# Kernel tuning notes

Hardware: AMD Instinct MI355X
Metric: run time of the kernel (lower is better)

Reference implementation:

```python
import jax, jax.numpy as jnp
import numpy as np

B, N, D = 8, 4096, 256
T = 768          # text_dim
E = 4            # num_experts
K = 2            # top_k
GS = 64          # grid_size = img_size // patch_size
WS = 8           # swin window size
NH = 4           # swin heads
MODES = 16       # fno modes
HID = 4 * D      # mlp hidden


def setup_inputs() -> dict:
    key = jax.random.key(0)
    ks = jax.random.split(key, 40)
    rn = lambda k, s, sc=0.02: jax.random.normal(k, s, jnp.float32) * sc
    return {
        "x": jax.random.normal(ks[0], (B, N, D), jnp.float32),
        "text_embedding": jax.random.normal(ks[1], (B, T), jnp.float32),
        # TopKGating: Linear(D+T->D), ReLU, Linear(D->E)
        "g1_w": rn(ks[2], (D, D + T)), "g1_b": jnp.zeros((D,), jnp.float32),
        "g2_w": rn(ks[3], (E, D)), "g2_b": jnp.zeros((E,), jnp.float32),
        # FNOExpert: SpectralConv2d complex weights (real/imag) + 1x1 conv
        "fno_w1r": rn(ks[4], (D, D, MODES, MODES), 1.0 / D), "fno_w1i": rn(ks[5], (D, D, MODES, MODES), 1.0 / D),
        "fno_w2r": rn(ks[6], (D, D, MODES, MODES), 1.0 / D), "fno_w2i": rn(ks[7], (D, D, MODES, MODES), 1.0 / D),
        "fno_cw": rn(ks[8], (D, D)), "fno_cb": jnp.zeros((D,), jnp.float32),
        # MLPExpert #1
        "m1_w1": rn(ks[9], (HID, D)), "m1_b1": jnp.zeros((HID,), jnp.float32),
        "m1_w2": rn(ks[10], (D, HID)), "m1_b2": jnp.zeros((D,), jnp.float32),
        # WindowAttentionExpert
        "a_ln1w": jnp.ones((D,), jnp.float32), "a_ln1b": jnp.zeros((D,), jnp.float32),
        "a_qkvw": rn(ks[11], (3 * D, D)), "a_qkvb": jnp.zeros((3 * D,), jnp.float32),
        "a_ow": rn(ks[12], (D, D)), "a_ob": jnp.zeros((D,), jnp.float32),
        "a_ln2w": jnp.ones((D,), jnp.float32), "a_ln2b": jnp.zeros((D,), jnp.float32),
        "a_mw1": rn(ks[13], (HID, D)), "a_mb1": jnp.zeros((HID,), jnp.float32),
        "a_mw2": rn(ks[14], (D, HID)), "a_mb2": jnp.zeros((D,), jnp.float32),
        # MLPExpert #2 (extra expert to reach num_experts=4)
        "m2_w1": rn(ks[15], (HID, D)), "m2_b1": jnp.zeros((HID,), jnp.float32),
        "m2_w2": rn(ks[16], (D, HID)), "m2_b2": jnp.zeros((D,), jnp.float32),
    }


def _gelu(v):
    return jax.nn.gelu(v, approximate=False)


def _ln(v, g, b, eps=1e-5):
    m = v.mean(-1, keepdims=True)
    var = ((v - m) ** 2).mean(-1, keepdims=True)
    return (v - m) * jax.lax.rsqrt(var + eps) * g + b


def reference(x, text_embedding, g1_w, g1_b, g2_w, g2_b,
              fno_w1r, fno_w1i, fno_w2r, fno_w2i, fno_cw, fno_cb,
              m1_w1, m1_b1, m1_w2, m1_b2,
              a_ln1w, a_ln1b, a_qkvw, a_qkvb, a_ow, a_ob,
              a_ln2w, a_ln2b, a_mw1, a_mb1, a_mw2, a_mb2,
              m2_w1, m2_b1, m2_w2, m2_b2):
    Bb, Nn, Dd = x.shape

    # ---- TopKGating ----
    feat = jnp.concatenate([x.mean(axis=1), text_embedding], axis=1)   # [B, D+T]
    h = jax.nn.relu(feat @ g1_w.T + g1_b)
    logits = h @ g2_w.T + g2_b                                         # [B, E]
    vals, idx = jax.lax.top_k(logits, K)
    w = jax.nn.softmax(vals, axis=1)                                   # [B, K]
    # per-(sample, expert) combine weight; indices are constants
    combine = (w[..., None] * jax.nn.one_hot(idx, E, dtype=x.dtype)).sum(axis=1)  # [B, E]

    # ---- Expert 0: FNO ----
    def fno(v):
        xg = v.transpose(0, 2, 1).reshape(Bb, Dd, GS, GS)              # [B, D, H, W]
        xft = jnp.fft.rfft2(xg)                                        # [B, D, H, W//2+1]
        w1 = fno_w1r + 1j * fno_w1i
        w2 = fno_w2r + 1j * fno_w2i
        lo = jnp.einsum('bixy,ioxy->boxy', xft[:, :, :MODES, :MODES], w1)
        hi = jnp.einsum('bixy,ioxy->boxy', xft[:, :, -MODES:, :MODES], w2)
        out_ft = jnp.zeros_like(xft)
        out_ft = out_ft.at[:, :, :MODES, :MODES].set(lo)
        out_ft = out_ft.at[:, :, -MODES:, :MODES].set(hi)
        x1 = jnp.fft.irfft2(out_ft, s=(GS, GS))
        x2 = jnp.einsum('bihw,oi->bohw', xg, fno_cw) + fno_cb[None, :, None, None]
        out = _gelu(x1 + x2)
        return out.reshape(Bb, Dd, Nn).transpose(0, 2, 1) + v

    # ---- MLP experts ----
    def mlp(v, w1, b1, w2, b2):
        return _gelu(v @ w1.T + b1) @ w2.T + b2 + v

    # ---- Expert 2: window attention ----
    def win_attn(v):
        xs = _ln(v, a_ln1w, a_ln1b).reshape(Bb, GS, GS, Dd)
        nw = GS // WS
        xw = xs.reshape(Bb, nw, WS, nw, WS, Dd).transpose(0, 1, 3, 2, 4, 5)
        xw = xw.reshape(-1, WS * WS, Dd)                               # [B*nw*nw, L, D]
        qkv = xw @ a_qkvw.T + a_qkvb
        q, k, vv = jnp.split(qkv, 3, axis=-1)
        dh = Dd // NH
        heads = lambda t: t.reshape(-1, WS * WS, NH, dh).transpose(0, 2, 1, 3)
        q, k, vv = heads(q), heads(k), heads(vv)
        attn = jax.nn.softmax(q @ k.transpose(0, 1, 3, 2) / jnp.sqrt(jnp.float32(dh)), axis=-1)
        o = (attn @ vv).transpose(0, 2, 1, 3).reshape(-1, WS * WS, Dd) @ a_ow.T + a_ob
        o = o.reshape(Bb, nw, nw, WS, WS, Dd).transpose(0, 1, 3, 2, 4, 5).reshape(Bb, Nn, Dd)
        v2 = v + o
        return v2 + (_gelu(_ln(v2, a_ln2w, a_ln2b) @ a_mw1.T + a_mb1) @ a_mw2.T + a_mb2)

    outs = [fno(x),
            mlp(x, m1_w1, m1_b1, m1_w2, m1_b2),
            win_attn(x),
            mlp(x, m2_w1, m2_b1, m2_w2, m2_b2)]
    final = sum(combine[:, e, None, None] * outs[e] for e in range(E))
    return final, w
```

## Files before the change

### kernel.cpp

```cpp
#include <hip/hip_runtime.h>
#include <math.h>

#define BB 8
#define NN 4096
#define DDIM 256
#define TT 768
#define BND (BB*NN*DDIM)

typedef unsigned short ushort_t;
typedef short bf16x8 __attribute__((ext_vector_type(8)));
typedef float f32x4 __attribute__((ext_vector_type(4)));

__device__ __forceinline__ float gelu_f(float v){
    return 0.5f * v * (1.0f + erff(v * 0.70710678118654752f));
}
__device__ __forceinline__ ushort_t f2bf(float f){
    union { float f; unsigned int u; } v; v.f = f;
    unsigned int u = v.u;
    u += 0x7FFFu + ((u >> 16) & 1u);
    return (ushort_t)(u >> 16);
}
__device__ __forceinline__ float bf2f(ushort_t h){
    union { unsigned int u; float f; } v; v.u = ((unsigned int)h) << 16;
    return v.f;
}
__device__ __forceinline__ float pk_re(unsigned int p){
    union { unsigned int u; float f; } v; v.u = p << 16; return v.f;
}
__device__ __forceinline__ float pk_im(unsigned int p){
    union { unsigned int u; float f; } v; v.u = p & 0xffff0000u; return v.f;
}
#define GLOAD16(gp, lp) __builtin_amdgcn_global_load_lds( \
    (__attribute__((address_space(1))) const void*)(gp),  \
    (__attribute__((address_space(3))) void*)(lp), 16, 0, 0)

__global__ __launch_bounds__(256) void k_meanA(const float* __restrict__ x, float* __restrict__ partial){
    int c = blockIdx.x, b = blockIdx.y, t = threadIdx.x;
    const float* p = x + ((size_t)b*NN + c*256)*DDIM + t;
    float s0=0,s1=0,s2=0,s3=0;
    for (int n=0;n<256;n+=4){
        s0 += p[(size_t)n*DDIM];
        s1 += p[(size_t)(n+1)*DDIM];
        s2 += p[(size_t)(n+2)*DDIM];
        s3 += p[(size_t)(n+3)*DDIM];
    }
    partial[((size_t)b*16 + c)*256 + t] = (s0+s1)+(s2+s3);
}

__global__ __launch_bounds__(256) void k_gate1(const float* __restrict__ partial, const float* __restrict__ text,
    const float* __restrict__ g1w, const float* __restrict__ g1b, float* __restrict__ hs){
    int d = blockIdx.x, t = threadIdx.x;
    int w = t >> 6, lane = t & 63;
    float xm[BB];
    #pragma unroll
    for (int b=0;b<BB;++b){
        float s = 0.f;
        #pragma unroll
        for (int c=0;c<16;++c) s += partial[((size_t)b*16 + c)*256 + t];
        xm[b] = s * (1.0f/NN);
    }
    const float* wrow = g1w + (size_t)d*(DDIM+TT);
    float w0 = wrow[t], w1 = wrow[256+t], w2 = wrow[512+t], w3 = wrow[768+t];
    float acc[BB];
    #pragma unroll
    for (int b=0;b<BB;++b){
        const float* tx = text + (size_t)b*TT;
        acc[b] = xm[b]*w0 + tx[t]*w1 + tx[256+t]*w2 + tx[512+t]*w3;
    }
    #pragma unroll
    for (int b=0;b<BB;++b)
        for (int off=32; off; off>>=1) acc[b] += __shfl_down(acc[b], off);
    __shared__ float red[BB][4];
    if (lane==0)
        #pragma unroll
        for (int b=0;b<BB;++b) red[b][w] = acc[b];
    __syncthreads();
    if (t < BB){
        float s = red[t][0]+red[t][1]+red[t][2]+red[t][3] + g1b[d];
        hs[t*DDIM + d] = fmaxf(s, 0.0f);
    }
}

__global__ __launch_bounds__(64) void k_gate2(const float* __restrict__ hs,
    const float* __restrict__ g2w, const float* __restrict__ g2b,
    float* __restrict__ combine, float* __restrict__ wout){
    __shared__ float lg[BB][4];
    int t = threadIdx.x;
    if (t < 32){
        int b = t>>2, e = t&3;
        float a = g2b[e];
        const float* w2 = g2w + e*DDIM;
        const float* h = hs + b*DDIM;
        for (int o=0;o<DDIM;o+=4)
            a += h[o]*w2[o] + h[o+1]*w2[o+1] + h[o+2]*w2[o+2] + h[o+3]*w2[o+3];
        lg[b][e] = a;
    }
    __syncthreads();
    if (t < BB){
        int b = t;
        int i1=0; float v1=lg[b][0];
        for (int e=1;e<4;++e){ if (lg[b][e] > v1){ v1=lg[b][e]; i1=e; } }
        int i2=0; float v2=-3.0e38f; bool found=false;
        for (int e=0;e<4;++e){ if (e==i1) continue; if (!found || lg[b][e] > v2){ v2=lg[b][e]; i2=e; found=true; } }
        float e2 = expf(v2 - v1);
        float inv = 1.0f/(1.0f + e2);
        float w0 = inv, w1 = e2*inv;
        float cv[4] = {0.f,0.f,0.f,0.f};
        cv[i1] = w0; cv[i2] = w1;
        for (int e=0;e<4;++e) combine[b*4+e] = cv[e];
        wout[b*2+0] = w0; wout[b*2+1] = w1;
    }
}

__global__ __launch_bounds__(256) void k_cvtw(
    const float* __restrict__ s0, const float* __restrict__ s1, const float* __restrict__ s2,
    const float* __restrict__ s3, const float* __restrict__ s4, const float* __restrict__ s5,
    const float* __restrict__ s6, const float* __restrict__ s7, const float* __restrict__ s8,
    ushort_t* __restrict__ dst){
    const int off[10] = {0,196608,262144,524288,786432,1048576,1310720,1572864,1835008,1900544};
    const float* srcs[9] = {s0,s1,s2,s3,s4,s5,s6,s7,s8};
    int i = (blockIdx.x*256 + threadIdx.x)*8;
    if (i >= 1900544) return;
    int seg = 0;
    #pragma unroll
    for (int k=1;k<9;++k) if (i >= off[k]) seg = k;
    const float* s = srcs[seg] + (i - off[seg]);
    ushort_t* d = dst + i;
    #pragma unroll
    for (int u=0;u<8;++u) d[u] = f2bf(s[u]);
}

__global__ __launch_bounds__(256) void k_xcvt2(const float4* __restrict__ x,
    const float* __restrict__ lng, const float* __restrict__ lnb,
    ushort_t* __restrict__ xbf, ushort_t* __restrict__ xlnbf, float4* __restrict__ outp){
    int w = threadIdx.x >> 6, lane = threadIdx.x & 63;
    int row = blockIdx.x*4 + w;
    size_t i4 = (size_t)row*64 + lane;
    float4 v = x[i4];
    outp[i4] = v;
    float vv[4] = {v.x, v.y, v.z, v.w};
    float s = (vv[0]+vv[1])+(vv[2]+vv[3]);
    float s2 = (vv[0]*vv[0]+vv[1]*vv[1])+(vv[2]*vv[2]+vv[3]*vv[3]);
    for (int off=32; off; off>>=1){ s += __shfl_down(s, off); s2 += __shfl_down(s2, off); }
    float m = __shfl(s, 0) * (1.0f/DDIM);
    float var = __shfl(s2, 0) * (1.0f/DDIM) - m*m;
    float r = rsqrtf(var + 1e-5f);
    int c0 = lane*4;
    #pragma unroll
    for (int u=0;u<4;++u){
        size_t i = i4*4 + u;
        xbf[i] = f2bf(vv[u]);
        xlnbf[i] = f2bf((vv[u]-m)*r*lng[c0+u] + lnb[c0+u]);
    }
}

__global__ __launch_bounds__(256) void k_v2cvt2(const float4* __restrict__ v2,
    const float* __restrict__ lng, const float* __restrict__ lnb,
    ushort_t* __restrict__ dstbf, const float* __restrict__ combine){
    int w = threadIdx.x >> 6, lane = threadIdx.x & 63;
    int row = blockIdx.x*4 + w;
    if (combine[(row>>12)*4+2]==0.0f) return;
    size_t i4 = (size_t)row*64 + lane;
    float4 v = v2[i4];
    float vv[4] = {v.x, v.y, v.z, v.w};
    float s = (vv[0]+vv[1])+(vv[2]+vv[3]);
    float s2 = (vv[0]*vv[0]+vv[1]*vv[1])+(vv[2]*vv[2]+vv[3]*vv[3]);
    for (int off=32; off; off>>=1){ s += __shfl_down(s, off); s2 += __shfl_down(s2, off); }
    float m = __shfl(s, 0) * (1.0f/DDIM);
    float var = __shfl(s2, 0) * (1.0f/DDIM) - m*m;
    float r = rsqrtf(var + 1e-5f);
    int c0 = lane*4;
    #pragma unroll
    for (int u=0;u<4;++u)
        dstbf[i4*4+u] = f2bf((vv[u]-m)*r*lng[c0+u] + lnb[c0+u]);
}

__global__ __launch_bounds__(256) void k_fft_w2(const float* __restrict__ x, float* __restrict__ F1,
                                                const float* __restrict__ combine){
    int h = blockIdx.x, b = blockIdx.y;
    if (combine[b*4+0]==0.0f) return;
    __shared__ float img[64*256];
    __shared__ float ct[64], st[64];
    int t = threadIdx.x;
    if (t < 64){ float ang = (float)t * 0.09817477042468103f; ct[t]=cosf(ang); st[t]=sinf(ang); }
    {
        const float4* src = (const float4*)(x + ((size_t)b*NN + h*64)*DDIM);
        float4* dst4 = (float4*)img;
        for (int i=t; i<4096; i+=256) dst4[i] = src[i];
    }
    __syncthreads();
    float re[16], im[16];
    #pragma unroll
    for (int ky=0;ky<16;++ky){ re[ky]=0.f; im[ky]=0.f; }
    for (int w=0; w<64; ++w){
        float v = img[w*256 + t];
        #pragma unroll
        for (int ky=0; ky<16; ++ky){
            int m = (ky*w)&63;
            re[ky] += v*ct[m];
            im[ky] -= v*st[m];
        }
    }
    float2* o = (float2*)(F1 + (((size_t)(b*DDIM + t))*1024 + h*16)*2);
    #pragma unroll
    for (int ky=0;ky<16;++ky) o[ky] = make_float2(re[ky], im[ky]);
}

__global__ __launch_bounds__(256) void k_fft_h(const float* __restrict__ F1,
                                               unsigned int* __restrict__ F2pk,
                                               const float* __restrict__ combine){
    int bd = blockIdx.x; int b = bd>>8;
    if (combine[b*4+0]==0.0f) return;
    __shared__ float f1[2048];
    __shared__ float ct[64], st[64];
    int t = threadIdx.x;
    if (t < 64){ float ang = (float)t * 0.09817477042468103f; ct[t]=cosf(ang); st[t]=sinf(ang); }
    const float* src = F1 + (size_t)bd*2048;
    for (int i=t;i<2048;i+=256) f1[i]=src[i];
    __syncthreads();
    for (int task=t; task<512; task+=256){
        int c = task>>8, kxp = (task>>4)&15, ky = task&15;
        int kx = c ? 48+kxp : kxp;
        float re=0.f, im=0.f;
        #pragma unroll
        for (int h=0;h<64;++h){
            int m = (kx*h)&63;
            float ar = f1[(h*16+ky)*2], ai = f1[(h*16+ky)*2+1];
            re += ar*ct[m] + ai*st[m];
            im += ai*ct[m] - ar*st[m];
        }
        F2pk[(size_t)bd*512 + task] = (((unsigned int)f2bf(im)) << 16) | (unsigned int)f2bf(re);
    }
}

__global__ __launch_bounds__(256) void k_specmul4(const unsigned int* __restrict__ F2pk,
    const float* __restrict__ w1r, const float* __restrict__ w1i,
    const float* __restrict__ w2r, const float* __restrict__ w2i,
    float* __restrict__ Gp, const float* __restrict__ combine){
    bool any=false;
    for (int b=0;b<BB;++b) any = any || (combine[b*4]!=0.0f);
    if (!any) return;
    int t  = threadIdx.x;
    int o0 = blockIdx.x * 2;
    int c  = blockIdx.y;
    int s  = blockIdx.z;
    const float* Wr = c ? w2r : w1r;
    const float* Wi = c ? w2i : w1i;
    float ar[2][BB], ai[2][BB];
    #pragma unroll
    for (int oo=0;oo<2;++oo)
        #pragma unroll
        for (int b=0;b<BB;++b){ ar[oo][b]=0.f; ai[oo][b]=0.f; }
    int i0 = s*64;
    for (int ii=i0; ii<i0+64; ii+=2){
        float wr[2][2], wi[2][2];
        #pragma unroll
        for (int u=0;u<2;++u)
            #pragma unroll
            for (int oo=0;oo<2;++oo){
                size_t widx = ((size_t)(ii+u)*DDIM + o0+oo)*256 + t;
                wr[u][oo] = Wr[widx];
                wi[u][oo] = Wi[widx];
            }
        unsigned int f[2][BB];
        #pragma unroll
        for (int u=0;u<2;++u)
            #pragma unroll
            for (int b=0;b<BB;++b)
                f[u][b] = F2pk[(size_t)b*131072 + (size_t)(ii+u)*512 + c*256 + t];
        #pragma unroll
        for (int u=0;u<2;++u)
            #pragma unroll
            for (int oo=0;oo<2;++oo)
                #pragma unroll
                for (int b=0;b<BB;++b){
                    float fr = pk_re(f[u][b]);
                    float fi = pk_im(f[u][b]);
                    ar[oo][b] += fr*wr[u][oo] - fi*wi[u][oo];
                    ai[oo][b] += fr*wi[u][oo] + fi*wr[u][oo];
                }
    }
    #pragma unroll
    for (int oo=0;oo<2;++oo)
        for (int b=0;b<BB;++b){
            float2* g = (float2*)(Gp + ((((size_t)s*BB + b)*DDIM + o0+oo)*512 + c*256 + t)*2);
            *g = make_float2(ar[oo][b], ai[oo][b]);
        }
}

__global__ __launch_bounds__(256) void k_ifft_h(const float* __restrict__ Gp, float* __restrict__ Z,
                                                const float* __restrict__ combine){
    int bd = blockIdx.x; int b = bd>>8;
    if (combine[b*4+0]==0.0f) return;
    __shared__ float g[1024];
    __shared__ float ct[64], st[64];
    int t=threadIdx.x;
    if (t < 64){ float ang = (float)t * 0.09817477042468103f; ct[t]=cosf(ang); st[t]=sinf(ang); }
    {
        const f32x4* p0 = (const f32x4*)(Gp + (size_t)bd*1024);
        const f32x4* p1 = (const f32x4*)(Gp + 2097152 + (size_t)bd*1024);
        const f32x4* p2 = (const f32x4*)(Gp + 2*2097152 + (size_t)bd*1024);
        const f32x4* p3 = (const f32x4*)(Gp + (size_t)3*2097152 + (size_t)bd*1024);
        f32x4 v = p0[t] + p1[t] + p2[t] + p3[t];
        *(f32x4*)(g + t*4) = v;
    }
    __syncthreads();
    for (int task=t;task<1024;task+=256){
        int h=task>>4, ky=task&15;
        float re=0.f, im=0.f;
        #pragma unroll
        for (int c=0;c<2;++c){
            #pragma unroll
            for (int kxp=0;kxp<16;++kxp){
                int kx = c ? 48+kxp : kxp;
                int m = (kx*h)&63;
                int gi = (c*256 + kxp*16 + ky)*2;
                float gr=g[gi], gim=g[gi+1];
                re += gr*ct[m] - gim*st[m];
                im += gr*st[m] + gim*ct[m];
            }
        }
        float2* o = (float2*)(Z + ((size_t)bd*1024 + task)*2);
        *o = make_float2(re*(1.0f/64.0f), im*(1.0f/64.0f));
    }
}

__global__ __launch_bounds__(256) void k_fno_out(const float* __restrict__ Z, const ushort_t* __restrict__ X2,
    const float* __restrict__ combine, float* __restrict__ out){
    int h = blockIdx.x, b = blockIdx.y;
    float cb = combine[b*4];
    if (cb==0.0f) return;
    __shared__ float ct[64], st[64];
    int t = threadIdx.x;
    if (t < 64){ float ang = (float)t * 0.09817477042468103f; ct[t]=cosf(ang); st[t]=sinf(ang); }
    __syncthreads();
    float zr[16], zi[16];
    const float* zp = Z + (((size_t)(b*DDIM + t)*64 + h)*16)*2;
    #pragma unroll
    for (int ky=0;ky<16;++ky){
        float2 v = *(const float2*)(zp + ky*2);
        zr[ky]=v.x; zi[ky]=v.y;
    }
    for (int w=0;w<64;++w){
        float s = zr[0];
        #pragma unroll
        for (int ky=1;ky<16;++ky){
            int m = (ky*w)&63;
            s += 2.0f*(zr[ky]*ct[m] - zi[ky]*st[m]);
        }
        s *= (1.0f/64.0f);
        size_t idx = ((size_t)b*NN + h*64 + w)*DDIM + t;
        out[idx] += cb * gelu_f(s + bf2f(X2[idx]));
    }
}

template<int EPI>
__global__ __launch_bounds__(256) void k_bgemm(
    const ushort_t* __restrict__ A, const ushort_t* __restrict__ W, const float* __restrict__ bias,
    void* __restrict__ dst, const float* __restrict__ combine, int expert, int K, int N,
    const float* __restrict__ xres, float* __restrict__ out)
{
    int tiles_n = N >> 7;
    int tm = blockIdx.x / tiles_n, tn = blockIdx.x - tm*tiles_n;
    int row0 = tm << 7, col0 = tn << 7;
    float scale = combine[(row0>>12)*4 + expert];
    if (scale == 0.0f) return;
    __shared__ __align__(16) ushort_t As[8192];
    __shared__ __align__(16) ushort_t Bs[8192];
    int t = threadIdx.x;
    int w = t >> 6, lane = t & 63;
    int wr = w >> 1, wc = w & 1;
    int lrow = lane >> 3, lk8 = (lane & 7) * 8;
    f32x4 acc[4][4];
    #pragma unroll
    for (int m=0;m<4;++m)
        #pragma unroll
        for (int n=0;n<4;++n) acc[m][n] = (f32x4){0.f,0.f,0.f,0.f};
    int afr = lane & 15, akr = (lane >> 4) * 8;
    for (int k0=0; k0<K; k0+=64){
        #pragma unroll
        for (int it=0; it<4; ++it){
            int c = it*4 + w;
            const ushort_t* ga = A + (size_t)(row0 + c*8 + lrow)*K + k0 + lk8;
            GLOAD16(ga, As + c*512);
            const ushort_t* gb = W + (size_t)(col0 + c*8 + lrow)*K + k0 + lk8;
            GLOAD16(gb, Bs + c*512);
        }
        __syncthreads();
        #pragma unroll
        for (int kk=0; kk<2; ++kk){
            bf16x8 af[4], bfr[4];
            #pragma unroll
            for (int m=0;m<4;++m)
                af[m] = *(const bf16x8*)(As + (wr*64 + m*16 + afr)*64 + kk*32 + akr);
            #pragma unroll
            for (int n=0;n<4;++n)
                bfr[n] = *(const bf16x8*)(Bs + (wc*64 + n*16 + afr)*64 + kk*32 + akr);
            #pragma unroll
            for (int m=0;m<4;++m)
                #pragma unroll
                for (int n=0;n<4;++n)
                    acc[m][n] = __builtin_amdgcn_mfma_f32_16x16x32_bf16(af[m], bfr[n], acc[m][n], 0, 0, 0);
        }
        __syncthreads();
    }
    int rbase = row0 + wr*64 + (lane>>4)*4;
    int cbase = col0 + wc*64 + (lane&15);
    #pragma unroll
    for (int n=0;n<4;++n){
        int col = cbase + n*16;
        float bcol = bias[col];
        #pragma unroll
        for (int m=0;m<4;++m){
            int r0 = rbase + m*16;
            f32x4 a = acc[m][n];
            #pragma unroll
            for (int j=0;j<4;++j){
                int r = r0 + j;
                float v = a[j] + bcol;
                if (EPI==0)      ((ushort_t*)dst)[(size_t)r*N + col] = f2bf(v);
                else if (EPI==1) ((ushort_t*)dst)[(size_t)r*N + col] = f2bf(gelu_f(v));
                else if (EPI==2) out[(size_t)r*DDIM + col] += scale * v;
                else if (EPI==3){
                    ((float*)dst)[(size_t)r*DDIM + col] = xres[(size_t)r*DDIM + col] + v;
                    out[(size_t)r*DDIM + col] += scale * v;
                }
            }
        }
    }
}

__global__ __launch_bounds__(256) void k_attn(const ushort_t* __restrict__ QKV, ushort_t* __restrict__ O,
                                              const float* __restrict__ combine){
    int wh = blockIdx.x;
    int w = wh>>2, head = wh&3;
    int b = w>>6;
    if (combine[b*4+2]==0.0f) return;
    int i1 = (w>>3)&7, i2 = w&7;
    __shared__ float A1[64][64];
    __shared__ float kk[64][65];
    __shared__ float S[64][65];
    int t = threadIdx.x;
    for (int idx=t; idx<4096; idx+=256){
        int l = idx>>6, dc = idx&63;
        int n = b*NN + (i1*8 + (l>>3))*64 + i2*8 + (l&7);
        const ushort_t* qrow = QKV + (size_t)n*768;
        A1[l][dc] = bf2f(qrow[head*64+dc]);
        kk[l][dc] = bf2f(qrow[256+head*64+dc]);
    }
    __syncthreads();
    for (int idx=t; idx<4096; idx+=256){
        int i=idx>>6, j=idx&63;
        float s=0.f;
        #pragma unroll 8
        for (int dc=0;dc<64;++dc) s += A1[i][dc]*kk[j][dc];
        S[i][j] = s * 0.125f;
    }
    __syncthreads();
    for (int idx=t; idx<4096; idx+=256){
        int l = idx>>6, dc = idx&63;
        int n = b*NN + (i1*8 + (l>>3))*64 + i2*8 + (l&7);
        A1[l][dc] = bf2f(QKV[(size_t)n*768 + 512 + head*64 + dc]);
    }
    __syncthreads();
    if (t < 64){
        float mx = -3.0e38f;
        for (int j=0;j<64;++j) mx = fmaxf(mx, S[t][j]);
        float sum=0.f;
        for (int j=0;j<64;++j){ float e = expf(S[t][j]-mx); S[t][j]=e; sum+=e; }
        float inv = 1.0f/sum;
        for (int j=0;j<64;++j) S[t][j] *= inv;
    }
    __syncthreads();
    for (int idx=t; idx<4096; idx+=256){
        int i=idx>>6, dc=idx&63;
        float s=0.f;
        #pragma unroll 8
        for (int j=0;j<64;++j) s += S[i][j]*A1[j][dc];
        int n = b*NN + (i1*8 + (i>>3))*64 + i2*8 + (i&7);
        O[(size_t)n*DDIM + head*64 + dc] = f2bf(s);
    }
}

extern "C" void kernel_launch(void* const* d_in, const int* in_sizes, int n_in,
                              void* d_out, int out_size, void* d_ws, size_t ws_size,
                              hipStream_t stream) {
    (void)in_sizes; (void)n_in; (void)out_size; (void)ws_size;
    const float* x      = (const float*)d_in[0];
    const float* text   = (const float*)d_in[1];
    const float* g1_w   = (const float*)d_in[2];
    const float* g1_b   = (const float*)d_in[3];
    const float* g2_w   = (const float*)d_in[4];
    const float* g2_b   = (const float*)d_in[5];
    const float* w1r    = (const float*)d_in[6];
    const float* w1i    = (const float*)d_in[7];
    const float* w2r    = (const float*)d_in[8];
    const float* w2i    = (const float*)d_in[9];
    const float* fno_cw = (const float*)d_in[10];
    const float* fno_cb = (const float*)d_in[11];
    const float* m1_w1  = (const float*)d_in[12];
    const float* m1_b1  = (const float*)d_in[13];
    const float* m1_w2  = (const float*)d_in[14];
    const float* m1_b2  = (const float*)d_in[15];
    const float* a_ln1w = (const float*)d_in[16];
    const float* a_ln1b = (const float*)d_in[17];
    const float* a_qkvw = (const float*)d_in[18];
    const float* a_qkvb = (const float*)d_in[19];
    const float* a_ow   = (const float*)d_in[20];
    const float* a_ob   = (const float*)d_in[21];
    const float* a_ln2w = (const float*)d_in[22];
    const float* a_ln2b = (const float*)d_in[23];
    const float* a_mw1  = (const float*)d_in[24];
    const float* a_mb1  = (const float*)d_in[25];
    const float* a_mw2  = (const float*)d_in[26];
    const float* a_mb2  = (const float*)d_in[27];
    const float* m2_w1  = (const float*)d_in[28];
    const float* m2_b1  = (const float*)d_in[29];
    const float* m2_w2  = (const float*)d_in[30];
    const float* m2_b2  = (const float*)d_in[31];

    float* out  = (float*)d_out;
    float* wout = out + (size_t)BND;

    float* wsf     = (float*)d_ws;
    float* hs      = wsf;
    float* combine = wsf + 2048;
    ushort_t* wbf  = (ushort_t*)(wsf + 69632);
    float* partial = wsf + 1019904;
    ushort_t* x_bf   = (ushort_t*)(wsf + 1118208);
    ushort_t* xln_bf = (ushort_t*)(wsf + 5312512);
    float* R1 = wsf + 9506816;
    float* Gp  = R1;
    float* F1  = R1 + 8388608;
    float* Z   = R1 + 16777216;
    ushort_t* X2_bf = (ushort_t*)(R1 + 20971520);
    unsigned int* F2pk = (unsigned int*)(R1 + 29360128);
    ushort_t* QKV_bf  = (ushort_t*)R1;
    ushort_t* O_bf    = (ushort_t*)(R1 + 12582912);
    float*    V2      = R1 + 16777216;
    ushort_t* v2ln_bf = (ushort_t*)(R1 + 25165824);
    ushort_t* H_bf = (ushort_t*)R1;

    ushort_t* qkvw_bf = wbf + 0;
    ushort_t* ow_bf   = wbf + 196608;
    ushort_t* mw1_bf  = wbf + 262144;
    ushort_t* mw2_bf  = wbf + 524288;
    ushort_t* m1w1_bf = wbf + 786432;
    ushort_t* m1w2_bf = wbf + 1048576;
    ushort_t* m2w1_bf = wbf + 1310720;
    ushort_t* m2w2_bf = wbf + 1572864;
    ushort_t* cw_bf   = wbf + 1835008;

    k_meanA<<<dim3(16,BB), 256, 0, stream>>>(x, partial);
    k_gate1<<<256, 256, 0, stream>>>(partial, text, g1_w, g1_b, hs);
    k_gate2<<<1, 64, 0, stream>>>(hs, g2_w, g2_b, combine, wout);
    k_cvtw<<<928, 256, 0, stream>>>(a_qkvw, a_ow, a_mw1, a_mw2, m1_w1, m1_w2, m2_w1, m2_w2, fno_cw, wbf);
    k_xcvt2<<<8192, 256, 0, stream>>>((const float4*)x, a_ln1w, a_ln1b, x_bf, xln_bf, (float4*)out);

    k_fft_w2<<<dim3(64,BB), 256, 0, stream>>>(x, F1, combine);
    k_fft_h<<<2048, 256, 0, stream>>>(F1, F2pk, combine);
    k_specmul4<<<dim3(128,2,4), 256, 0, stream>>>(F2pk, w1r, w1i, w2r, w2i, Gp, combine);
    k_ifft_h<<<2048, 256, 0, stream>>>(Gp, Z, combine);
    k_bgemm<0><<<512, 256, 0, stream>>>(x_bf, cw_bf, fno_cb, X2_bf, combine, 0, 256, 256, nullptr, nullptr);
    k_fno_out<<<dim3(64,8), 256, 0, stream>>>(Z, X2_bf, combine, out);

    k_bgemm<1><<<2048, 256, 0, stream>>>(x_bf, m1w1_bf, m1_b1, H_bf, combine, 1, 256, 1024, nullptr, nullptr);
    k_bgemm<2><<<512, 256, 0, stream>>>(H_bf, m1w2_bf, m1_b2, nullptr, combine, 1, 1024, 256, nullptr, out);

    k_bgemm<0><<<1536, 256, 0, stream>>>(xln_bf, qkvw_bf, a_qkvb, QKV_bf, combine, 2, 256, 768, nullptr, nullptr);
    k_attn<<<2048, 256, 0, stream>>>(QKV_bf, O_bf, combine);
    k_bgemm<3><<<512, 256, 0, stream>>>(O_bf, ow_bf, a_ob, V2, combine, 2, 256, 256, x, out);
    k_v2cvt2<<<8192, 256, 0, stream>>>((const float4*)V2, a_ln2w, a_ln2b, v2ln_bf, combine);
    k_bgemm<1><<<2048, 256, 0, stream>>>(v2ln_bf, mw1_bf, a_mb1, H_bf, combine, 2, 256, 1024, nullptr, nullptr);
    k_bgemm<2><<<512, 256, 0, stream>>>(H_bf, mw2_bf, a_mb2, nullptr, combine, 2, 1024, 256, nullptr, out);

    k_bgemm<1><<<2048, 256, 0, stream>>>(x_bf, m2w1_bf, m2_b1, H_bf, combine, 3, 256, 1024, nullptr, nullptr);
    k_bgemm<2><<<512, 256, 0, stream>>>(H_bf, m2w2_bf, m2_b2, nullptr, combine, 3, 1024, 256, nullptr, out);
}
```

Before: 627.8 us.

## Fuse token-mean partial sums into x conversion, read bf16 x in FFT, unroll specmul

The gating mean over tokens is now computed inside the x conversion/LayerNorm kernel. Each block writes a 4-row partial sum and a small k_meanB kernel reduces them, so the separate full pass over x in k_meanA goes away. The width FFT now reads the bf16 copy of x instead of fp32, which halves its load traffic and shared-memory footprint but drops input precision for the FNO path. The spectral multiply loop is unrolled over 4 input channels instead of 2 to expose more loads in flight, at the cost of extra registers.

```diff
diff --git a/kernel.cpp b/kernel.cpp
--- a/kernel.cpp
+++ b/kernel.cpp
@@ -34,17 +34,55 @@
     (__attribute__((address_space(1))) const void*)(gp),  \
     (__attribute__((address_space(3))) void*)(lp), 16, 0, 0)
 
-__global__ __launch_bounds__(256) void k_meanA(const float* __restrict__ x, float* __restrict__ partial){
-    int c = blockIdx.x, b = blockIdx.y, t = threadIdx.x;
-    const float* p = x + ((size_t)b*NN + c*256)*DDIM + t;
+__global__ __launch_bounds__(256) void k_xcvt2(const float4* __restrict__ x,
+    const float* __restrict__ lng, const float* __restrict__ lnb,
+    ushort_t* __restrict__ xbf, ushort_t* __restrict__ xlnbf, float4* __restrict__ outp,
+    float* __restrict__ partialA){
+    int w = threadIdx.x >> 6, lane = threadIdx.x & 63;
+    int row = blockIdx.x*4 + w;
+    size_t i4 = (size_t)row*64 + lane;
+    float4 v = x[i4];
+    outp[i4] = v;
+    float vv[4] = {v.x, v.y, v.z, v.w};
+    __shared__ float sda[4][256];
+    *(float4*)&sda[w][lane*4] = v;
+    float s = (vv[0]+vv[1])+(vv[2]+vv[3]);
+    float s2 = (vv[0]*vv[0]+vv[1]*vv[1])+(vv[2]*vv[2]+vv[3]*vv[3]);
+    for (int off=32; off; off>>=1){ s += __shfl_down(s, off); s2 += __shfl_down(s2, off); }
+    float m = __shfl(s, 0) * (1.0f/DDIM);
+    float var = __shfl(s2, 0) * (1.0f/DDIM) - m*m;
+    float r = rsqrtf(var + 1e-5f);
+    int c0 = lane*4;
+    #pragma unroll
+    for (int u=0;u<4;++u){
+        size_t i = i4*4 + u;
+        xbf[i] = f2bf(vv[u]);
+        xlnbf[i] = f2bf((vv[u]-m)*r*lng[c0+u] + lnb[c0+u]);
+    }
+    __syncthreads();
+    if (w==0){
+        float4 a = *(const float4*)&sda[0][lane*4];
+        float4 b4 = *(const float4*)&sda[1][lane*4];
+        float4 c4 = *(const float4*)&sda[2][lane*4];
+        float4 d4 = *(const float4*)&sda[3][lane*4];
+        float4 sum = make_float4(a.x+b4.x+c4.x+d4.x, a.y+b4.y+c4.y+d4.y,
+                                 a.z+b4.z+c4.z+d4.z, a.w+b4.w+c4.w+d4.w);
+        *(float4*)&partialA[(size_t)blockIdx.x*256 + lane*4] = sum;
+    }
+}
+
+__global__ __launch_bounds__(256) void k_meanB(const float* __restrict__ partialA, float* __restrict__ partialB){
+    int seg = blockIdx.x, b = blockIdx.y, t = threadIdx.x;
+    const float* p = partialA + ((size_t)(b*1024 + seg*64))*256 + t;
     float s0=0,s1=0,s2=0,s3=0;
-    for (int n=0;n<256;n+=4){
-        s0 += p[(size_t)n*DDIM];
-        s1 += p[(size_t)(n+1)*DDIM];
-        s2 += p[(size_t)(n+2)*DDIM];
-        s3 += p[(size_t)(n+3)*DDIM];
-    }
-    partial[((size_t)b*16 + c)*256 + t] = (s0+s1)+(s2+s3);
+    #pragma unroll
+    for (int c=0;c<64;c+=4){
+        s0 += p[(size_t)c*256];
+        s1 += p[(size_t)(c+1)*256];
+        s2 += p[(size_t)(c+2)*256];
+        s3 += p[(size_t)(c+3)*256];
+    }
+    partialB[((size_t)b*16 + seg)*256 + t] = (s0+s1)+(s2+s3);
 }
 
 __global__ __launch_bounds__(256) void k_gate1(const float* __restrict__ partial, const float* __restrict__ text,
@@ -128,30 +166,6 @@
     ushort_t* d = dst + i;
     #pragma unroll
     for (int u=0;u<8;++u) d[u] = f2bf(s[u]);
-}
-
-__global__ __launch_bounds__(256) void k_xcvt2(const float4* __restrict__ x,
-    const float* __restrict__ lng, const float* __restrict__ lnb,
-    ushort_t* __restrict__ xbf, ushort_t* __restrict__ xlnbf, float4* __restrict__ outp){
-    int w = threadIdx.x >> 6, lane = threadIdx.x & 63;
-    int row = blockIdx.x*4 + w;
-    size_t i4 = (size_t)row*64 + lane;
-    float4 v = x[i4];
-    outp[i4] = v;
-    float vv[4] = {v.x, v.y, v.z, v.w};
-    float s = (vv[0]+vv[1])+(vv[2]+vv[3]);
-    float s2 = (vv[0]*vv[0]+vv[1]*vv[1])+(vv[2]*vv[2]+vv[3]*vv[3]);
-    for (int off=32; off; off>>=1){ s += __shfl_down(s, off); s2 += __shfl_down(s2, off); }
-    float m = __shfl(s, 0) * (1.0f/DDIM);
-    float var = __shfl(s2, 0) * (1.0f/DDIM) - m*m;
-    float r = rsqrtf(var + 1e-5f);
-    int c0 = lane*4;
-    #pragma unroll
-    for (int u=0;u<4;++u){
-        size_t i = i4*4 + u;
-        xbf[i] = f2bf(vv[u]);
-        xlnbf[i] = f2bf((vv[u]-m)*r*lng[c0+u] + lnb[c0+u]);
-    }
 }
 
 __global__ __launch_bounds__(256) void k_v2cvt2(const float4* __restrict__ v2,
@@ -175,25 +189,25 @@
         dstbf[i4*4+u] = f2bf((vv[u]-m)*r*lng[c0+u] + lnb[c0+u]);
 }
 
-__global__ __launch_bounds__(256) void k_fft_w2(const float* __restrict__ x, float* __restrict__ F1,
+__global__ __launch_bounds__(256) void k_fft_w2(const ushort_t* __restrict__ xbf, float* __restrict__ F1,
                                                 const float* __restrict__ combine){
     int h = blockIdx.x, b = blockIdx.y;
     if (combine[b*4+0]==0.0f) return;
-    __shared__ float img[64*256];
+    __shared__ ushort_t img[64*256];
     __shared__ float ct[64], st[64];
     int t = threadIdx.x;
     if (t < 64){ float ang = (float)t * 0.09817477042468103f; ct[t]=cosf(ang); st[t]=sinf(ang); }
     {
-        const float4* src = (const float4*)(x + ((size_t)b*NN + h*64)*DDIM);
-        float4* dst4 = (float4*)img;
-        for (int i=t; i<4096; i+=256) dst4[i] = src[i];
+        const uint4* src = (const uint4*)(xbf + ((size_t)b*NN + h*64)*DDIM);
+        uint4* dst4 = (uint4*)img;
+        for (int i=t; i<2048; i+=256) dst4[i] = src[i];
     }
     __syncthreads();
     float re[16], im[16];
     #pragma unroll
     for (int ky=0;ky<16;++ky){ re[ky]=0.f; im[ky]=0.f; }
     for (int w=0; w<64; ++w){
-        float v = img[w*256 + t];
+        float v = bf2f(img[w*256 + t]);
         #pragma unroll
         for (int ky=0; ky<16; ++ky){
             int m = (ky*w)&63;
@@ -252,24 +266,24 @@
         #pragma unroll
         for (int b=0;b<BB;++b){ ar[oo][b]=0.f; ai[oo][b]=0.f; }
     int i0 = s*64;
-    for (int ii=i0; ii<i0+64; ii+=2){
-        float wr[2][2], wi[2][2];
-        #pragma unroll
-        for (int u=0;u<2;++u)
+    for (int ii=i0; ii<i0+64; ii+=4){
+        float wr[4][2], wi[4][2];
+        #pragma unroll
+        for (int u=0;u<4;++u)
             #pragma unroll
             for (int oo=0;oo<2;++oo){
                 size_t widx = ((size_t)(ii+u)*DDIM + o0+oo)*256 + t;
                 wr[u][oo] = Wr[widx];
                 wi[u][oo] = Wi[widx];
             }
-        unsigned int f[2][BB];
-        #pragma unroll
-        for (int u=0;u<2;++u)
+        unsigned int f[4][BB];
+        #pragma unroll
+        for (int u=0;u<4;++u)
             #pragma unroll
             for (int b=0;b<BB;++b)
                 f[u][b] = F2pk[(size_t)b*131072 + (size_t)(ii+u)*512 + c*256 + t];
         #pragma unroll
-        for (int u=0;u<2;++u)
+        for (int u=0;u<4;++u)
             #pragma unroll
             for (int oo=0;oo<2;++oo)
                 #pragma unroll
@@ -526,10 +540,11 @@
     float* hs      = wsf;
     float* combine = wsf + 2048;
     ushort_t* wbf  = (ushort_t*)(wsf + 69632);
-    float* partial = wsf + 1019904;
+    float* partialB = wsf + 1019904;
     ushort_t* x_bf   = (ushort_t*)(wsf + 1118208);
     ushort_t* xln_bf = (ushort_t*)(wsf + 5312512);
     float* R1 = wsf + 9506816;
+    float* partialA = R1;
     float* Gp  = R1;
     float* F1  = R1 + 8388608;
     float* Z   = R1 + 16777216;
@@ -551,13 +566,13 @@
     ushort_t* m2w2_bf = wbf + 1572864;
     ushort_t* cw_bf   = wbf + 1835008;
 
-    k_meanA<<<dim3(16,BB), 256, 0, stream>>>(x, partial);
-    k_gate1<<<256, 256, 0, stream>>>(partial, text, g1_w, g1_b, hs);
+    k_xcvt2<<<8192, 256, 0, stream>>>((const float4*)x, a_ln1w, a_ln1b, x_bf, xln_bf, (float4*)out, partialA);
+    k_meanB<<<dim3(16,BB), 256, 0, stream>>>(partialA, partialB);
+    k_gate1<<<256, 256, 0, stream>>>(partialB, text, g1_w, g1_b, hs);
     k_gate2<<<1, 64, 0, stream>>>(hs, g2_w, g2_b, combine, wout);
     k_cvtw<<<928, 256, 0, stream>>>(a_qkvw, a_ow, a_mw1, a_mw2, m1_w1, m1_w2, m2_w1, m2_w2, fno_cw, wbf);
-    k_xcvt2<<<8192, 256, 0, stream>>>((const float4*)x, a_ln1w, a_ln1b, x_bf, xln_bf, (float4*)out);
-
-    k_fft_w2<<<dim3(64,BB), 256, 0, stream>>>(x, F1, combine);
+
+    k_fft_w2<<<dim3(64,BB), 256, 0, stream>>>(x_bf, F1, combine);
     k_fft_h<<<2048, 256, 0, stream>>>(F1, F2pk, combine);
     k_specmul4<<<dim3(128,2,4), 256, 0, stream>>>(F2pk, w1r, w1i, w2r, w2i, Gp, combine);
     k_ifft_h<<<2048, 256, 0, stream>>>(Gp, Z, combine);
```

Measured after the change: 605.6 us. -3.5%, faster.
